# Optimization experiments

Hardware: AMD Instinct MI355X
Metric: run time of the kernel (lower is better)

Reference implementation:

```python
import jax, jax.numpy as jnp
import numpy as np
from math import gcd

N_SIG = 2097152   # signal length
L_FILT = 129      # FIR taps


def setup_inputs() -> dict:
    key = jax.random.key(0)
    k1, k2 = jax.random.split(key)
    x = jax.random.normal(k1, (N_SIG,), dtype=jnp.float32)
    h = jax.random.normal(k2, (L_FILT,), dtype=jnp.float32)
    return {"x": x, "h": h, "up": 3, "down": 2}


def _get_start_index(length):
    if length <= 2:
        return 0
    return (length - 1) // 2


def reference(x, h, up, down):
    # Reduce rates by gcd, as in the torch module.
    g = gcd(up, down)
    up, down = up // g, down // g
    if up == 1 and down == 1:
        return x
    N = x.shape[0]
    L = h.shape[0]
    # zero-stuff: x_up[::up] = up * x  (gain `up` matches resample_poly)
    x_up = jnp.zeros(up * N, dtype=x.dtype).at[::up].set(up * x)
    # full FIR convolution, then phase-offset strided downsample
    full = jnp.convolve(x_up, h.astype(x.dtype), mode="full")  # [up*N + L - 1]
    start = _get_start_index(L)
    n_out = -(-(N * up) // down)  # ceil(N*up/down)
    return full[start::down][:n_out]
```

## Files before the change

kernel.cpp:

```cpp
#include <hip/hip_runtime.h>


#define N_SIG   2097152
#define L_FILT  129
#define G       2
#define BLK     128
#define GPB     (BLK * G)
#define OPB     (3 * GPB)
#define TILE_Q  560

template <int I0>
__device__ __forceinline__ void load_win8(const float* __restrict__ xs, int tid,
                                          float (&wz)[12]) {
    const float4* p = (const float4*)(xs + 4 * tid + (40 - I0));
    const float4 a = p[0], b = p[1], c = p[2];
    wz[0] = a.x; wz[1]  = a.y; wz[2]  = a.z; wz[3]  = a.w;
    wz[4] = b.x; wz[5]  = b.y; wz[6]  = b.z; wz[7]  = b.w;
    wz[8] = c.x; wz[9]  = c.y; wz[10] = c.z; wz[11] = c.w;
}

template <int I0>
__device__ __forceinline__ void fma8(const float* __restrict__ h,
                                     const float (&wz)[12], float (&acc)[6]) {
#pragma unroll
    for (int u = 0; u < 8; ++u) {
        const float h0 = h[3 * (I0 + u) + 0];
        const float h1 = h[3 * (I0 + u) + 1];
        const float h2 = h[3 * (I0 + u) + 2];
#pragma unroll
        for (int g = 0; g < 2; ++g) {
            const float xa = wz[7 - u + 2 * g];
            const float xb = wz[8 - u + 2 * g];
            acc[3 * g + 0] += xa * h1;
            acc[3 * g + 1] += xb * h0;
            acc[3 * g + 2] += xb * h2;
        }
    }
}

__device__ __forceinline__ void load_tail(const float* __restrict__ xs, int tid,
                                          float (&wt)[8]) {
    const float4* p = (const float4*)(xs + 4 * tid + 4);
    const float4 a = p[0], b = p[1];
    wt[0] = a.x; wt[1] = a.y; wt[2] = a.z; wt[3] = a.w;
    wt[4] = b.x; wt[5] = b.y; wt[6] = b.z; wt[7] = b.w;
}

__device__ __forceinline__ void fma_tail(const float* __restrict__ h,
                                         const float (&wt)[8], float (&acc)[6]) {
#pragma unroll
    for (int u = 0; u < 3; ++u) {
        const float h0 = h[3 * (40 + u) + 0];
        const float h1 = h[3 * (40 + u) + 1];
        const float h2 = h[3 * (40 + u) + 2];
#pragma unroll
        for (int g = 0; g < 2; ++g) {
            const float xa = wt[3 - u + 2 * g];
            const float xb = wt[4 - u + 2 * g];
            acc[3 * g + 0] += xa * h1;
            acc[3 * g + 1] += xb * h0;
            acc[3 * g + 2] += xb * h2;
        }
    }
}

__global__ __launch_bounds__(BLK, 6) void poly_kernel(
    const float* __restrict__ x, const float* __restrict__ h,
    float* __restrict__ out, int nblocks)
{
    __shared__ alignas(16) float xs[TILE_Q];

    const int tid = threadIdx.x;
    const int b   = blockIdx.x;
    const int tb  = 512 * b - 26;

    if (b != 0 && b != nblocks - 1) {
        {
            const float* g0 = x + (tb + 4 * tid);
            const float2 lo = *(const float2*)(g0);
            const float2 hi = *(const float2*)(g0 + 2);
            *(float4*)(xs + 4 * tid) = make_float4(lo.x, lo.y, hi.x, hi.y);
        }
        if (tid < TILE_Q / 4 - BLK) {
            const float* g0 = x + (tb + 4 * (BLK + tid));
            const float2 lo = *(const float2*)(g0);
            const float2 hi = *(const float2*)(g0 + 2);
            *(float4*)(xs + 4 * (BLK + tid)) = make_float4(lo.x, lo.y, hi.x, hi.y);
        }
    } else {
        for (int q4 = tid; q4 < TILE_Q / 4; q4 += BLK) {
            const int gx = tb + 4 * q4;
            float4 v;
            v.x = (gx     >= 0 && gx     < N_SIG) ? x[gx]     : 0.0f;
            v.y = (gx + 1 >= 0 && gx + 1 < N_SIG) ? x[gx + 1] : 0.0f;
            v.z = (gx + 2 >= 0 && gx + 2 < N_SIG) ? x[gx + 2] : 0.0f;
            v.w = (gx + 3 >= 0 && gx + 3 < N_SIG) ? x[gx + 3] : 0.0f;
            *(float4*)(xs + 4 * q4) = v;
        }
    }
    __syncthreads();

    float acc[6] = {0.f, 0.f, 0.f, 0.f, 0.f, 0.f};

    float wA[12], wB[12], wC[12], wT[8];
    load_win8<0>(xs, tid, wA);
    load_win8<8>(xs, tid, wB);
    load_win8<16>(xs, tid, wC);
    fma8<0>(h, wA, acc);
    load_win8<24>(xs, tid, wA);
    fma8<8>(h, wB, acc);
    load_win8<32>(xs, tid, wB);
    fma8<16>(h, wC, acc);
    load_tail(xs, tid, wT);
    fma8<24>(h, wA, acc);
    fma8<32>(h, wB, acc);
    fma_tail(h, wT, acc);

    const int ob = OPB * b + 6 * tid;
    *(float2*)(out + ob + 0) = make_float2(3.0f * acc[0], 3.0f * acc[1]);
    *(float2*)(out + ob + 2) = make_float2(3.0f * acc[2], 3.0f * acc[3]);
    *(float2*)(out + ob + 4) = make_float2(3.0f * acc[4], 3.0f * acc[5]);
}

extern "C" void kernel_launch(void* const* d_in, const int* in_sizes, int n_in,
                              void* d_out, int out_size, void* d_ws, size_t ws_size,
                              hipStream_t stream) {
    const float* x = (const float*)d_in[0];
    const float* h = (const float*)d_in[1];
    float* out = (float*)d_out;
    const int blocks = (out_size + OPB - 1) / OPB;
    poly_kernel<<<blocks, BLK, 0, stream>>>(x, h, out, blocks);
}
```

Before: 73.39 us.

## Load FIR window directly from global into registers, drop shared-memory staging

Removes the shared-memory tile and __syncthreads. Each thread now reads its 52-sample window straight from global memory into registers as 13 float4 loads, relying on L1/L2 to serve the heavy overlap between neighbouring threads. Block size doubles to 256 with matching per-block indexing, and outputs use nontemporal stores. This cuts LDS traffic and the barrier, but raises register pressure (a 52-float array) and redundant global/L1 traffic, and occupancy may drop.

Measured after the change: 71.29 us. -2.9%, faster.

```diff
diff --git a/kernel.cpp b/kernel.cpp
--- a/kernel.cpp
+++ b/kernel.cpp
@@ -2,26 +2,18 @@
 
 
 #define N_SIG   2097152
-#define L_FILT  129
 #define G       2
-#define BLK     128
+#define BLK     256
 #define GPB     (BLK * G)
 #define OPB     (3 * GPB)
-#define TILE_Q  560
+#define NW      52
 
-template <int I0>
-__device__ __forceinline__ void load_win8(const float* __restrict__ xs, int tid,
-                                          float (&wz)[12]) {
-    const float4* p = (const float4*)(xs + 4 * tid + (40 - I0));
-    const float4 a = p[0], b = p[1], c = p[2];
-    wz[0] = a.x; wz[1]  = a.y; wz[2]  = a.z; wz[3]  = a.w;
-    wz[4] = b.x; wz[5]  = b.y; wz[6]  = b.z; wz[7]  = b.w;
-    wz[8] = c.x; wz[9]  = c.y; wz[10] = c.z; wz[11] = c.w;
-}
+typedef float v2f __attribute__((ext_vector_type(2)));
+
 
 template <int I0>
 __device__ __forceinline__ void fma8(const float* __restrict__ h,
-                                     const float (&wz)[12], float (&acc)[6]) {
+                                     const float (&w)[NW], float (&acc)[6]) {
 #pragma unroll
     for (int u = 0; u < 8; ++u) {
         const float h0 = h[3 * (I0 + u) + 0];
@@ -29,8 +21,8 @@
         const float h2 = h[3 * (I0 + u) + 2];
 #pragma unroll
         for (int g = 0; g < 2; ++g) {
-            const float xa = wz[7 - u + 2 * g];
-            const float xb = wz[8 - u + 2 * g];
+            const float xa = w[45 - (I0 + u) + 2 * g];
+            const float xb = w[46 - (I0 + u) + 2 * g];
             acc[3 * g + 0] += xa * h1;
             acc[3 * g + 1] += xb * h0;
             acc[3 * g + 2] += xb * h2;
@@ -38,16 +30,38 @@
     }
 }
 
-__device__ __forceinline__ void load_tail(const float* __restrict__ xs, int tid,
-                                          float (&wt)[8]) {
-    const float4* p = (const float4*)(xs + 4 * tid + 4);
-    const float4 a = p[0], b = p[1];
-    wt[0] = a.x; wt[1] = a.y; wt[2] = a.z; wt[3] = a.w;
-    wt[4] = b.x; wt[5] = b.y; wt[6] = b.z; wt[7] = b.w;
-}
+__global__ __launch_bounds__(BLK, 4) void poly_kernel(
+    const float* __restrict__ x, const float* __restrict__ h,
+    float* __restrict__ out, int nblocks)
+{
+    const int tid = threadIdx.x;
+    const int b   = blockIdx.x;
 
-__device__ __forceinline__ void fma_tail(const float* __restrict__ h,
-                                         const float (&wt)[8], float (&acc)[6]) {
+    const long base = (long)1024 * b + 4 * tid - 24;
+
+    float w[NW];
+    if (b != 0 && b != nblocks - 1) {
+        const float4* p = (const float4*)(x + base);
+#pragma unroll
+        for (int k = 12; k >= 0; --k) {
+            const float4 v = p[k];
+            w[4 * k + 0] = v.x; w[4 * k + 1] = v.y;
+            w[4 * k + 2] = v.z; w[4 * k + 3] = v.w;
+        }
+    } else {
+#pragma unroll
+        for (int k = 0; k < NW; ++k) {
+            const long gi = base + k;
+            w[k] = (gi >= 0 && gi < N_SIG) ? x[gi] : 0.0f;
+        }
+    }
+
+    float acc[6] = {0.f, 0.f, 0.f, 0.f, 0.f, 0.f};
+    fma8<0 >(h, w, acc);
+    fma8<8 >(h, w, acc);
+    fma8<16>(h, w, acc);
+    fma8<24>(h, w, acc);
+    fma8<32>(h, w, acc);
 #pragma unroll
     for (int u = 0; u < 3; ++u) {
         const float h0 = h[3 * (40 + u) + 0];
@@ -55,71 +69,21 @@
         const float h2 = h[3 * (40 + u) + 2];
 #pragma unroll
         for (int g = 0; g < 2; ++g) {
-            const float xa = wt[3 - u + 2 * g];
-            const float xb = wt[4 - u + 2 * g];
+            const float xa = w[5 - u + 2 * g];
+            const float xb = w[6 - u + 2 * g];
             acc[3 * g + 0] += xa * h1;
             acc[3 * g + 1] += xb * h0;
             acc[3 * g + 2] += xb * h2;
         }
     }
-}
-
-__global__ __launch_bounds__(BLK, 6) void poly_kernel(
-    const float* __restrict__ x, const float* __restrict__ h,
-    float* __restrict__ out, int nblocks)
-{
-    __shared__ alignas(16) float xs[TILE_Q];
-
-    const int tid = threadIdx.x;
-    const int b   = blockIdx.x;
-    const int tb  = 512 * b - 26;
-
-    if (b != 0 && b != nblocks - 1) {
-        {
-            const float* g0 = x + (tb + 4 * tid);
-            const float2 lo = *(const float2*)(g0);
-            const float2 hi = *(const float2*)(g0 + 2);
-            *(float4*)(xs + 4 * tid) = make_float4(lo.x, lo.y, hi.x, hi.y);
-        }
-        if (tid < TILE_Q / 4 - BLK) {
-            const float* g0 = x + (tb + 4 * (BLK + tid));
-            const float2 lo = *(const float2*)(g0);
-            const float2 hi = *(const float2*)(g0 + 2);
-            *(float4*)(xs + 4 * (BLK + tid)) = make_float4(lo.x, lo.y, hi.x, hi.y);
-        }
-    } else {
-        for (int q4 = tid; q4 < TILE_Q / 4; q4 += BLK) {
-            const int gx = tb + 4 * q4;
-            float4 v;
-            v.x = (gx     >= 0 && gx     < N_SIG) ? x[gx]     : 0.0f;
-            v.y = (gx + 1 >= 0 && gx + 1 < N_SIG) ? x[gx + 1] : 0.0f;
-            v.z = (gx + 2 >= 0 && gx + 2 < N_SIG) ? x[gx + 2] : 0.0f;
-            v.w = (gx + 3 >= 0 && gx + 3 < N_SIG) ? x[gx + 3] : 0.0f;
-            *(float4*)(xs + 4 * q4) = v;
-        }
-    }
-    __syncthreads();
-
-    float acc[6] = {0.f, 0.f, 0.f, 0.f, 0.f, 0.f};
-
-    float wA[12], wB[12], wC[12], wT[8];
-    load_win8<0>(xs, tid, wA);
-    load_win8<8>(xs, tid, wB);
-    load_win8<16>(xs, tid, wC);
-    fma8<0>(h, wA, acc);
-    load_win8<24>(xs, tid, wA);
-    fma8<8>(h, wB, acc);
-    load_win8<32>(xs, tid, wB);
-    fma8<16>(h, wC, acc);
-    load_tail(xs, tid, wT);
-    fma8<24>(h, wA, acc);
-    fma8<32>(h, wB, acc);
-    fma_tail(h, wT, acc);
 
     const int ob = OPB * b + 6 * tid;
-    *(float2*)(out + ob + 0) = make_float2(3.0f * acc[0], 3.0f * acc[1]);
-    *(float2*)(out + ob + 2) = make_float2(3.0f * acc[2], 3.0f * acc[3]);
-    *(float2*)(out + ob + 4) = make_float2(3.0f * acc[4], 3.0f * acc[5]);
+    v2f s0; s0.x = 3.0f * acc[0]; s0.y = 3.0f * acc[1];
+    v2f s1; s1.x = 3.0f * acc[2]; s1.y = 3.0f * acc[3];
+    v2f s2; s2.x = 3.0f * acc[4]; s2.y = 3.0f * acc[5];
+    __builtin_nontemporal_store(s0, (v2f*)(out + ob + 0));
+    __builtin_nontemporal_store(s1, (v2f*)(out + ob + 2));
+    __builtin_nontemporal_store(s2, (v2f*)(out + ob + 4));
 }
 
 extern "C" void kernel_launch(void* const* d_in, const int* in_sizes, int n_in,
```
